# Kernel optimization log

Hardware: AMD Instinct MI355X
Metric: run time of the kernel (lower is better)

Reference implementation:

```python
import jax, jax.numpy as jnp
import numpy as np


def setup_inputs() -> dict:
    key = jax.random.key(0)
    k1, k2, k3, k4, k5 = jax.random.split(key, 5)
    in_f, out_f, rank = 4096, 4096, 16
    std = 1.0 / np.sqrt(rank)
    x = jax.random.normal(k1, (4, 2048, in_f), dtype=jnp.float32)
    base_weight = jax.random.normal(k2, (out_f, in_f), dtype=jnp.float32) * 0.02
    lora_A = jax.random.normal(k3, (rank, in_f), dtype=jnp.float32) * std
    lora_B = jax.random.normal(k4, (out_f, rank), dtype=jnp.float32) * 0.01
    magnitude_vec = jax.random.uniform(k5, (out_f,), dtype=jnp.float32) + 0.5
    return {"x": x, "base_weight": base_weight, "lora_A": lora_A,
            "lora_B": lora_B, "magnitude_vec": magnitude_vec}


def reference(x, base_weight, lora_A, lora_B, magnitude_vec):
    # x: [B, S, in] -> tokens [N, in]
    out_shape = (*x.shape[:-1], base_weight.shape[0])
    xt = x.reshape(-1, x.shape[-1])
    # low-rank adapter path: [N, rank] @ [rank, out]
    lora_out = (xt @ lora_A.T) @ lora_B.T
    # column-wise L2 norm of adapted weight, per output row: [out]
    adapted_w = base_weight + lora_B @ lora_A
    column_norm = jnp.linalg.norm(adapted_w, axis=1)
    magnitude_scale = magnitude_vec / column_norm  # [out]
    # base GEMM + adapter + magnitude rescale epilogue
    dora_out = (xt @ base_weight.T + lora_out) * magnitude_scale[None, :]
    return dora_out.reshape(out_shape)
```

## Files before the change

kernel.cpp:

```cpp
#include <hip/hip_runtime.h>
#include <hip/hip_bf16.h>
#include <stdint.h>

typedef __attribute__((ext_vector_type(8))) short s16x8;
typedef __attribute__((ext_vector_type(4))) float f32x4;
typedef __attribute__((ext_vector_type(4))) unsigned short us4;

__device__ inline unsigned short bf_rne(float f) {
    union { float f; uint32_t u; } v; v.f = f;
    uint32_t u = v.u;
    u += 0x7FFFu + ((u >> 16) & 1u);
    return (unsigned short)(u >> 16);
}

#define GLD_LDS16(gp, lp)                                                     \
    __builtin_amdgcn_global_load_lds(                                         \
        (const __attribute__((address_space(1))) void*)(gp),                  \
        (__attribute__((address_space(3))) void*)(lp), 16, 0, 0)

#define LDSOFF(p) ((unsigned)(uintptr_t)(__attribute__((address_space(3))) const void*)(p))

__global__ __launch_bounds__(256) void prologue_kernel(
    const float4* __restrict__ x4, us4* __restrict__ xbf4,
    const float4* __restrict__ W4,
    const float4* __restrict__ A4,
    const float* __restrict__ B,
    const float* __restrict__ mag,
    unsigned short* __restrict__ wbf,
    float* __restrict__ scale) {
    const int tid = threadIdx.x;
    if (blockIdx.x < 512) {
        const int m0 = blockIdx.x * 8;
        __shared__ float Bs[8][16];
        __shared__ float red[32];
        if (tid < 128) Bs[tid >> 4][tid & 15] = B[m0 * 16 + tid];
        __syncthreads();
        float ss[8] = {};
        for (int c = tid; c < 1024; c += 256) {
            float4 a[16];
#pragma unroll
            for (int r = 0; r < 16; ++r) a[r] = A4[r * 1024 + c];
#pragma unroll
            for (int i = 0; i < 8; ++i) {
                float4 w = W4[(size_t)(m0 + i) * 1024 + c];
#pragma unroll
                for (int r = 0; r < 16; ++r) {
                    const float br = Bs[i][r];
                    w.x += br * a[r].x; w.y += br * a[r].y;
                    w.z += br * a[r].z; w.w += br * a[r].w;
                }
                ss[i] += w.x * w.x + w.y * w.y + w.z * w.z + w.w * w.w;
                us4 o; o[0] = bf_rne(w.x); o[1] = bf_rne(w.y);
                o[2] = bf_rne(w.z); o[3] = bf_rne(w.w);
                *(us4*)&wbf[(size_t)(m0 + i) * 4096 + c * 4] = o;
            }
        }
        const int lane = tid & 63, wv = tid >> 6;
#pragma unroll
        for (int i = 0; i < 8; ++i) {
            float v = ss[i];
#pragma unroll
            for (int off = 32; off > 0; off >>= 1) v += __shfl_down(v, off, 64);
            if (lane == 0) red[wv * 8 + i] = v;
        }
        __syncthreads();
        if (tid < 8) {
            float tot = red[tid] + red[8 + tid] + red[16 + tid] + red[24 + tid];
            scale[m0 + tid] = mag[m0 + tid] / sqrtf(tot);
        }
    } else {
        const size_t base = (size_t)(blockIdx.x - 512) * 1024 + tid;
#pragma unroll
        for (int j = 0; j < 4; ++j) {
            const size_t idx = base + j * 256;
            float4 a = x4[idx];
            us4 o;
            o[0] = bf_rne(a.x); o[1] = bf_rne(a.y);
            o[2] = bf_rne(a.z); o[3] = bf_rne(a.w);
            xbf4[idx] = o;
        }
    }
}

#define FENCE() asm volatile("" ::: "memory")
#define BAR()   do { FENCE(); __builtin_amdgcn_s_barrier(); FENCE(); } while (0)
#define VMW6()  asm volatile("s_waitcnt vmcnt(6)" ::: "memory")
#define VMW0()  asm volatile("s_waitcnt vmcnt(0)" ::: "memory")
#define LGW0()  asm volatile("s_waitcnt lgkmcnt(0)" ::: "memory")
#define SB0()   __builtin_amdgcn_sched_barrier(0)
#define PRIO1() __builtin_amdgcn_s_setprio(1)
#define PRIO0() __builtin_amdgcn_s_setprio(0)

#define DSR(dst, va, IMM) \
    asm volatile("ds_read_b128 %0, %1 offset:" #IMM : "=v"(dst) : "v"(va))

__global__ __launch_bounds__(512, 2) void dora_gemm(
    const unsigned short* __restrict__ xbf,
    const unsigned short* __restrict__ wbf,
    const float* __restrict__ scale,
    float* __restrict__ out) {
    __shared__ __align__(16) unsigned short As[2][256 * 64];
    __shared__ __align__(16) unsigned short Bs[2][256 * 64];

    const int tid  = threadIdx.x;
    const int lane = tid & 63;
    const int w    = tid >> 6;
    const int wm   = w >> 2;
    const int wn   = w & 3;
    const int q    = lane >> 4;
    const int c15  = lane & 15;

    const int bid = blockIdx.x;
    const int xcd = bid & 7, sub = bid >> 3;
    const int tileM = (((xcd & 3) << 3) | (sub & 7)) << 8;
    const int tileN = (((xcd >> 2) << 3) | (sub >> 3)) << 8;

    const int r0 = tid >> 3;
    const int lc = (tid & 7) ^ (r0 & 7);
    const size_t aoff = (size_t)(tileM + r0) * 4096 + lc * 8;
    const size_t boff = (size_t)(tileN + r0) * 4096 + lc * 8;
    const int ld0 = (w * 64) * 8;
    const int ld1 = (512 + w * 64) * 8;

#define STAGE_A(d, h, k0) do {                                                            \
    GLD_LDS16(xbf + aoff + (size_t)((h) * 128) * 4096 + (k0),      &As[d][(h) * 8192 + ld0]); \
    GLD_LDS16(xbf + aoff + (size_t)((h) * 128 + 64) * 4096 + (k0), &As[d][(h) * 8192 + ld1]); \
} while (0)
#define STAGE_B(d, h, k0) do {                                                            \
    GLD_LDS16(wbf + boff + (size_t)((h) * 128) * 4096 + (k0),      &Bs[d][(h) * 8192 + ld0]); \
    GLD_LDS16(wbf + boff + (size_t)((h) * 128 + 64) * 4096 + (k0), &Bs[d][(h) * 8192 + ld1]); \
} while (0)

    const int rb = c15 & 7;
    unsigned aA[4][2], aB[2][2];
#pragma unroll
    for (int mt = 0; mt < 4; ++mt)
#pragma unroll
        for (int kc = 0; kc < 2; ++kc)
            aA[mt][kc] = LDSOFF(&As[0][(wm * 64 + mt * 16 + c15) * 64 +
                                       ((kc * 4 + q) ^ rb) * 8]);
#pragma unroll
    for (int nt = 0; nt < 2; ++nt)
#pragma unroll
        for (int kc = 0; kc < 2; ++kc)
            aB[nt][kc] = LDSOFF(&Bs[0][(wn * 32 + nt * 16 + c15) * 64 +
                                       ((kc * 4 + q) ^ rb) * 8]);

    s16x8 af[4][2];
    s16x8 bfx[2][2][2];
    f32x4 acc[8][4] = {};

#define RD_A(IMM) do {                                                        \
    DSR(af[0][0], aA[0][0], IMM); DSR(af[0][1], aA[0][1], IMM);               \
    DSR(af[1][0], aA[1][0], IMM); DSR(af[1][1], aA[1][1], IMM);               \
    DSR(af[2][0], aA[2][0], IMM); DSR(af[2][1], aA[2][1], IMM);               \
    DSR(af[3][0], aA[3][0], IMM); DSR(af[3][1], aA[3][1], IMM); } while (0)
#define RD_B(nh, IMM) do {                                                    \
    DSR(bfx[nh][0][0], aB[0][0], IMM); DSR(bfx[nh][0][1], aB[0][1], IMM);     \
    DSR(bfx[nh][1][0], aB[1][0], IMM); DSR(bfx[nh][1][1], aB[1][1], IMM); } while (0)

#define MFMA_Q(mh, nh) do {                                                   \
    _Pragma("unroll") for (int mt = 0; mt < 4; ++mt)                          \
    _Pragma("unroll") for (int nt = 0; nt < 2; ++nt)                          \
    _Pragma("unroll") for (int kc = 0; kc < 2; ++kc)                          \
        acc[(mh) * 4 + mt][(nh) * 2 + nt] =                                   \
            __builtin_amdgcn_mfma_f32_16x16x32_bf16(                          \
                af[mt][kc], bfx[nh][nt][kc],                                  \
                acc[(mh) * 4 + mt][(nh) * 2 + nt], 0, 0, 0);                  \
} while (0)

    STAGE_A(0, 0, 0); STAGE_B(0, 0, 0); STAGE_B(0, 1, 0); STAGE_A(0, 1, 0);
    STAGE_A(1, 0, 64); STAGE_B(1, 0, 64); STAGE_B(1, 1, 64);
    VMW6(); BAR();

    for (int t0k = 0; t0k <= 60 * 64; t0k += 128) {
        const int kt1 = t0k + 64;
        const int kn2 = t0k + 128;
        const int kn3 = t0k + 192;
        RD_A(0); RD_B(0, 0);
        STAGE_A(1, 1, kt1);
        BAR(); LGW0(); SB0();
        PRIO1(); MFMA_Q(0, 0); PRIO0();
        RD_B(1, 16384);
        BAR(); LGW0(); SB0();
        PRIO1(); MFMA_Q(0, 1); PRIO0();
        RD_A(16384);
        STAGE_A(0, 0, kn2); STAGE_B(0, 0, kn2);
        BAR(); LGW0(); SB0();
        PRIO1(); MFMA_Q(1, 1); PRIO0();
        STAGE_B(0, 1, kn2);
        VMW6(); BAR();
        PRIO1(); MFMA_Q(1, 0); PRIO0();
        RD_A(32768); RD_B(0, 32768);
        STAGE_A(0, 1, kn2);
        BAR(); LGW0(); SB0();
        PRIO1(); MFMA_Q(0, 0); PRIO0();
        RD_B(1, 49152);
        BAR(); LGW0(); SB0();
        PRIO1(); MFMA_Q(0, 1); PRIO0();
        RD_A(49152);
        STAGE_A(1, 0, kn3); STAGE_B(1, 0, kn3);
        BAR(); LGW0(); SB0();
        PRIO1(); MFMA_Q(1, 1); PRIO0();
        STAGE_B(1, 1, kn3);
        VMW6(); BAR();
        PRIO1(); MFMA_Q(1, 0); PRIO0();
    }

    RD_A(0); RD_B(0, 0);
    STAGE_A(1, 1, 4032);
    BAR(); LGW0(); SB0();
    PRIO1(); MFMA_Q(0, 0); PRIO0();
    RD_B(1, 16384);
    BAR(); LGW0(); SB0();
    PRIO1(); MFMA_Q(0, 1); PRIO0();
    RD_A(16384);
    BAR(); LGW0(); SB0();
    PRIO1(); MFMA_Q(1, 1); PRIO0();
    VMW0(); BAR();
    PRIO1(); MFMA_Q(1, 0); PRIO0();
    RD_A(32768); RD_B(0, 32768);
    LGW0(); SB0();
    PRIO1(); MFMA_Q(0, 0); PRIO0();
    RD_B(1, 49152);
    LGW0(); SB0();
    PRIO1(); MFMA_Q(0, 1); PRIO0();
    RD_A(49152);
    LGW0(); SB0();
    PRIO1(); MFMA_Q(1, 1); MFMA_Q(1, 0); PRIO0();

#pragma unroll
    for (int nh = 0; nh < 2; ++nh)
#pragma unroll
    for (int nt = 0; nt < 2; ++nt) {
        const int col = tileN + nh * 128 + wn * 32 + nt * 16 + c15;
        const float s = scale[col];
#pragma unroll
        for (int mh = 0; mh < 2; ++mh)
#pragma unroll
        for (int mt = 0; mt < 4; ++mt) {
            const int row0 = tileM + mh * 128 + wm * 64 + mt * 16 + q * 4;
#pragma unroll
            for (int r = 0; r < 4; ++r)
                out[(size_t)(row0 + r) * 4096 + col] = acc[mh * 4 + mt][nh * 2 + nt][r] * s;
        }
    }
}

extern "C" void kernel_launch(void* const* d_in, const int* in_sizes, int n_in,
                              void* d_out, int out_size, void* d_ws, size_t ws_size,
                              hipStream_t stream) {
    const float* x   = (const float*)d_in[0];
    const float* W   = (const float*)d_in[1];
    const float* A   = (const float*)d_in[2];
    const float* B   = (const float*)d_in[3];
    const float* mag = (const float*)d_in[4];
    float* out = (float*)d_out;

    const size_t XBF_BYTES = (size_t)8192 * 4096 * 2;
    const size_t WBF_BYTES = (size_t)4096 * 4096 * 2;
    const size_t NEEDED = XBF_BYTES + WBF_BYTES + 4096 * sizeof(float);
    if (ws_size < NEEDED) return;

    unsigned short* xbf = (unsigned short*)d_ws;
    unsigned short* wbf = (unsigned short*)((char*)d_ws + XBF_BYTES);
    float* scale = (float*)((char*)d_ws + XBF_BYTES + WBF_BYTES);

    prologue_kernel<<<8704, 256, 0, stream>>>((const float4*)x, (us4*)xbf,
                                              (const float4*)W, (const float4*)A,
                                              B, mag, wbf, scale);
    dora_gemm<<<512, 512, 0, stream>>>(xbf, wbf, scale, out);
}
```

Before: 304.4 us.

## Restructure GEMM main loop into simpler per-tile double-buffered schedule

Replaces the finely interleaved 8-phase main loop, which issued partial stage loads between MFMA quarters with a barrier at each phase, with a per-tile macro. Each tile waits for all global loads, takes one barrier, issues the next tile's full stage into the other buffer, then runs the four MFMA quarters with partial lgkmcnt waits. This cuts the number of barriers per K-tile and simplifies dependencies. In exchange, the vmcnt(0) wait at each tile start exposes global-load latency more, since the prefetch distance drops to one tile.

```diff
diff --git a/kernel.cpp b/kernel.cpp
--- a/kernel.cpp
+++ b/kernel.cpp
@@ -84,9 +84,8 @@
 
 #define FENCE() asm volatile("" ::: "memory")
 #define BAR()   do { FENCE(); __builtin_amdgcn_s_barrier(); FENCE(); } while (0)
-#define VMW6()  asm volatile("s_waitcnt vmcnt(6)" ::: "memory")
-#define VMW0()  asm volatile("s_waitcnt vmcnt(0)" ::: "memory")
-#define LGW0()  asm volatile("s_waitcnt lgkmcnt(0)" ::: "memory")
+#define VMW(n)  asm volatile("s_waitcnt vmcnt(" #n ")" ::: "memory")
+#define LGW(n)  asm volatile("s_waitcnt lgkmcnt(" #n ")" ::: "memory")
 #define SB0()   __builtin_amdgcn_sched_barrier(0)
 #define PRIO1() __builtin_amdgcn_s_setprio(1)
 #define PRIO0() __builtin_amdgcn_s_setprio(0)
@@ -169,65 +168,33 @@
                 acc[(mh) * 4 + mt][(nh) * 2 + nt], 0, 0, 0);                  \
 } while (0)
 
+#define TILE1(IA0, IA1, IB0, IB1, DD, KN) do {                                \
+    VMW(0); BAR();                                                            \
+    STAGE_A(DD, 0, KN); STAGE_B(DD, 0, KN);                                   \
+    STAGE_B(DD, 1, KN); STAGE_A(DD, 1, KN);                                   \
+    RD_B(0, IB0); RD_A(IA0);                                                  \
+    RD_B(1, IB1);                                                             \
+    LGW(4); SB0(); PRIO1(); MFMA_Q(0, 0); PRIO0();                            \
+    LGW(0); SB0(); PRIO1(); MFMA_Q(0, 1); PRIO0();                            \
+    RD_A(IA1);                                                                \
+    LGW(0); SB0(); PRIO1(); MFMA_Q(1, 1); PRIO0();                            \
+    PRIO1(); MFMA_Q(1, 0); PRIO0();                                           \
+} while (0)
+
     STAGE_A(0, 0, 0); STAGE_B(0, 0, 0); STAGE_B(0, 1, 0); STAGE_A(0, 1, 0);
-    STAGE_A(1, 0, 64); STAGE_B(1, 0, 64); STAGE_B(1, 1, 64);
-    VMW6(); BAR();
-
-    for (int t0k = 0; t0k <= 60 * 64; t0k += 128) {
-        const int kt1 = t0k + 64;
-        const int kn2 = t0k + 128;
-        const int kn3 = t0k + 192;
-        RD_A(0); RD_B(0, 0);
-        STAGE_A(1, 1, kt1);
-        BAR(); LGW0(); SB0();
-        PRIO1(); MFMA_Q(0, 0); PRIO0();
-        RD_B(1, 16384);
-        BAR(); LGW0(); SB0();
-        PRIO1(); MFMA_Q(0, 1); PRIO0();
-        RD_A(16384);
-        STAGE_A(0, 0, kn2); STAGE_B(0, 0, kn2);
-        BAR(); LGW0(); SB0();
-        PRIO1(); MFMA_Q(1, 1); PRIO0();
-        STAGE_B(0, 1, kn2);
-        VMW6(); BAR();
-        PRIO1(); MFMA_Q(1, 0); PRIO0();
-        RD_A(32768); RD_B(0, 32768);
-        STAGE_A(0, 1, kn2);
-        BAR(); LGW0(); SB0();
-        PRIO1(); MFMA_Q(0, 0); PRIO0();
-        RD_B(1, 49152);
-        BAR(); LGW0(); SB0();
-        PRIO1(); MFMA_Q(0, 1); PRIO0();
-        RD_A(49152);
-        STAGE_A(1, 0, kn3); STAGE_B(1, 0, kn3);
-        BAR(); LGW0(); SB0();
-        PRIO1(); MFMA_Q(1, 1); PRIO0();
-        STAGE_B(1, 1, kn3);
-        VMW6(); BAR();
-        PRIO1(); MFMA_Q(1, 0); PRIO0();
+
+    for (int kn = 64; kn <= 3904; kn += 128) {
+        TILE1(0, 16384, 0, 16384, 1, kn);
+        TILE1(32768, 49152, 32768, 49152, 0, kn + 64);
     }
-
-    RD_A(0); RD_B(0, 0);
-    STAGE_A(1, 1, 4032);
-    BAR(); LGW0(); SB0();
-    PRIO1(); MFMA_Q(0, 0); PRIO0();
-    RD_B(1, 16384);
-    BAR(); LGW0(); SB0();
-    PRIO1(); MFMA_Q(0, 1); PRIO0();
-    RD_A(16384);
-    BAR(); LGW0(); SB0();
-    PRIO1(); MFMA_Q(1, 1); PRIO0();
-    VMW0(); BAR();
-    PRIO1(); MFMA_Q(1, 0); PRIO0();
-    RD_A(32768); RD_B(0, 32768);
-    LGW0(); SB0();
-    PRIO1(); MFMA_Q(0, 0); PRIO0();
+    TILE1(0, 16384, 0, 16384, 1, 4032);
+    VMW(0); BAR();
+    RD_B(0, 32768); RD_A(32768);
     RD_B(1, 49152);
-    LGW0(); SB0();
-    PRIO1(); MFMA_Q(0, 1); PRIO0();
+    LGW(4); SB0(); PRIO1(); MFMA_Q(0, 0); PRIO0();
+    LGW(0); SB0(); PRIO1(); MFMA_Q(0, 1); PRIO0();
     RD_A(49152);
-    LGW0(); SB0();
-    PRIO1(); MFMA_Q(1, 1); MFMA_Q(1, 0); PRIO0();
+    LGW(0); SB0(); PRIO1(); MFMA_Q(1, 1); MFMA_Q(1, 0); PRIO0();
 
 #pragma unroll
     for (int nh = 0; nh < 2; ++nh)
```

New measurement: 313.9 us. 3.1% more time.
